# Optimization experiments

Measured on AMD Instinct MI355X. Metric: run time of the kernel, lower is better.

The kernel has to match this reference:

```python
import jax, jax.numpy as jnp
import numpy as np

EPS = 1e-12


def agnn_layer(x, row, col, num_nodes):
    """AGNN propagation with beta frozen at 1.0 (requires_grad=False in source).
    alpha_ij = softmax_{j in N(i)} ( beta * cos(x_i, x_j) ); out_i = sum_j alpha_ij * x_j.
    row = destination node of each edge (segment id), col = source node.
    """
    xn = x / (jnp.linalg.norm(x, axis=-1, keepdims=True) + EPS)  # unit-norm features
    score = jnp.sum(xn[row] * xn[col], axis=-1)                   # [E] beta=1 * cos sim
    smax = jax.ops.segment_max(score, row, num_segments=num_nodes)
    e = jnp.exp(score - smax[row])                                # stable softmax numerator
    denom = jax.ops.segment_sum(e, row, num_segments=num_nodes)
    alpha = e / jnp.maximum(denom[row], EPS)                      # [E]
    out = jax.ops.segment_sum(alpha[:, None] * x[col], row, num_segments=num_nodes)
    return out


def setup_inputs() -> dict:
    key = jax.random.key(0)
    ks = jax.random.split(key, 8)
    N, E = 100000, 1600000
    IN_DIM, HID, OUT_DIM = 128, 64, 64
    x = jax.random.normal(ks[0], (N, IN_DIM), dtype=jnp.float32)
    edge_row = jnp.sort(jax.random.randint(ks[1], (E,), 0, N))
    edge_col = jax.random.randint(ks[2], (E,), 0, N)
    # Linear params (PyTorch nn.Linear style: y = x @ W.T + b)
    s1 = 1.0 / np.sqrt(IN_DIM)
    W1 = jax.random.uniform(ks[3], (HID, IN_DIM), jnp.float32, -s1, s1)
    b1 = jax.random.uniform(ks[4], (HID,), jnp.float32, -s1, s1)
    s2 = 1.0 / np.sqrt(HID)
    W2 = jax.random.uniform(ks[5], (OUT_DIM, HID), jnp.float32, -s2, s2)
    b2 = jax.random.uniform(ks[6], (OUT_DIM,), jnp.float32, -s2, s2)
    return {"x": x, "edge_row": edge_row, "edge_col": edge_col,
            "W1": W1, "b1": b1, "W2": W2, "b2": b2}


def reference(x, edge_row, edge_col, W1, b1, W2, b2):
    N = x.shape[0]
    h = jax.nn.relu(x @ W1.T + b1)
    for _ in range(4):  # 4 frozen-beta AGNN layers
        h = jax.nn.relu(agnn_layer(h, edge_row, edge_col, N))
    return h @ W2.T + b2
```

## Files before the change

kernel.cpp:

```cpp
#include <hip/hip_runtime.h>


typedef float v2f __attribute__((ext_vector_type(2)));

#define DEV_INLINE __device__ __forceinline__

DEV_INLINE v2f bf2(unsigned u) {
    v2f r;
    r.x = __uint_as_float(u << 16);
    r.y = __uint_as_float(u & 0xffff0000u);
    return r;
}

DEV_INLINE unsigned pack_bf16_2(float a, float b) {
    unsigned ua = __float_as_uint(a); ua += 0x7fffu + ((ua >> 16) & 1u);
    unsigned ub = __float_as_uint(b); ub += 0x7fffu + ((ub >> 16) & 1u);
    return (ua >> 16) | (ub & 0xffff0000u);
}

__global__ __launch_bounds__(256) void build_rowptr(const int* __restrict__ row,
                                                    int* __restrict__ ptr,
                                                    int N, int E) {
    int i = blockIdx.x * blockDim.x + threadIdx.x;
    if (i > N) return;
    int lo = 0, hi = E;
    while (lo < hi) {
        int mid = (lo + hi) >> 1;
        if (row[mid] < i) lo = mid + 1; else hi = mid;
    }
    ptr[i] = lo;
}

__global__ __launch_bounds__(256) void gemm1_relu(const float* __restrict__ x,
                                                  const float* __restrict__ W1,
                                                  const float* __restrict__ b1,
                                                  unsigned short* __restrict__ xn,
                                                  float* __restrict__ nrm,
                                                  int N) {
    __shared__ __align__(16) float Wt[128 * 64];
    __shared__ __align__(16) float xT[128 * 64];
    const int tid  = threadIdx.x;
    const int tx   = tid & 15;
    const int ty   = tid >> 4;
    const int base = blockIdx.x * 64;

    {
        const float4* W4 = (const float4*)W1;
        for (int idx = tid; idx < 128 * 16; idx += 256) {
            int o = idx & 63, k4 = idx >> 6;
            float4 v = W4[o * 32 + k4];
            Wt[(4 * k4 + 0) * 64 + o] = v.x;
            Wt[(4 * k4 + 1) * 64 + o] = v.y;
            Wt[(4 * k4 + 2) * 64 + o] = v.z;
            Wt[(4 * k4 + 3) * 64 + o] = v.w;
        }
        const float4* x4p = (const float4*)x;
        for (int idx = tid; idx < 128 * 16; idx += 256) {
            int mm = idx & 63, k4 = idx >> 6;
            int node = base + mm;
            float4 v = make_float4(0.f, 0.f, 0.f, 0.f);
            if (node < N) v = x4p[(size_t)node * 32 + k4];
            xT[(4 * k4 + 0) * 64 + mm] = v.x;
            xT[(4 * k4 + 1) * 64 + mm] = v.y;
            xT[(4 * k4 + 2) * 64 + mm] = v.z;
            xT[(4 * k4 + 3) * 64 + mm] = v.w;
        }
    }
    __syncthreads();

    float4 b4 = ((const float4*)b1)[tx];
    float4 acc[4];
    acc[0] = b4; acc[1] = b4; acc[2] = b4; acc[3] = b4;

#pragma unroll 4
    for (int k = 0; k < 128; ++k) {
        const float4 w4 = *(const float4*)&Wt[k * 64 + 4 * tx];
        const float4 xv = *(const float4*)&xT[k * 64 + 4 * ty];
        acc[0].x = fmaf(xv.x, w4.x, acc[0].x);
        acc[0].y = fmaf(xv.x, w4.y, acc[0].y);
        acc[0].z = fmaf(xv.x, w4.z, acc[0].z);
        acc[0].w = fmaf(xv.x, w4.w, acc[0].w);
        acc[1].x = fmaf(xv.y, w4.x, acc[1].x);
        acc[1].y = fmaf(xv.y, w4.y, acc[1].y);
        acc[1].z = fmaf(xv.y, w4.z, acc[1].z);
        acc[1].w = fmaf(xv.y, w4.w, acc[1].w);
        acc[2].x = fmaf(xv.z, w4.x, acc[2].x);
        acc[2].y = fmaf(xv.z, w4.y, acc[2].y);
        acc[2].z = fmaf(xv.z, w4.z, acc[2].z);
        acc[2].w = fmaf(xv.z, w4.w, acc[2].w);
        acc[3].x = fmaf(xv.w, w4.x, acc[3].x);
        acc[3].y = fmaf(xv.w, w4.y, acc[3].y);
        acc[3].z = fmaf(xv.w, w4.z, acc[3].z);
        acc[3].w = fmaf(xv.w, w4.w, acc[3].w);
    }

#pragma unroll
    for (int mm = 0; mm < 4; ++mm) {
        float4 r = acc[mm];
        r.x = fmaxf(r.x, 0.f); r.y = fmaxf(r.y, 0.f);
        r.z = fmaxf(r.z, 0.f); r.w = fmaxf(r.w, 0.f);
        float s = fmaf(r.x, r.x, fmaf(r.y, r.y, fmaf(r.z, r.z, r.w * r.w)));
        s += __shfl_xor(s, 1, 64);
        s += __shfl_xor(s, 2, 64);
        s += __shfl_xor(s, 4, 64);
        s += __shfl_xor(s, 8, 64);
        const float nn  = sqrtf(s) + 1e-12f;
        const float inv = 1.f / nn;
        int node = base + 4 * ty + mm;
        if (node < N) {
            uint2 pk;
            pk.x = pack_bf16_2(r.x * inv, r.y * inv);
            pk.y = pack_bf16_2(r.z * inv, r.w * inv);
            *(uint2*)&xn[(size_t)node * 64 + 4 * tx] = pk;
            if (tx == mm) nrm[node] = nn;
        }
    }
}

__global__ __launch_bounds__(256) void agnn_layer(const uint4* __restrict__ xn4,
                                                  const float* __restrict__ nrm,
                                                  const int* __restrict__ ptr,
                                                  const int* __restrict__ col,
                                                  uint4* __restrict__ xo4,
                                                  float* __restrict__ nrmo,
                                                  int N) {
    const int tid  = threadIdx.x;
    const int lane = tid & 63;
    const int g    = (lane >> 3) & 3;
    const int sub  = lane & 7;
    const int i    = blockIdx.x * 8 + (tid >> 5);
    if (i >= N) return;

    const float L2E = 1.4426950408889634f;
    const uint4 hv = xn4[(size_t)i * 8 + sub];
    v2f hi0 = bf2(hv.x), hi1 = bf2(hv.y), hi2v = bf2(hv.z), hi3 = bf2(hv.w);
    hi0 *= L2E; hi1 *= L2E; hi2v *= L2E; hi3 *= L2E;

    const int p0 = ptr[i], p1 = ptr[i + 1];

    float den = 0.f;
    v2f a0 = {0.f, 0.f}, a1 = {0.f, 0.f}, a2 = {0.f, 0.f}, a3 = {0.f, 0.f};

    int e = p0 + g;
    for (; e + 4 < p1; e += 8) {
        const int ja = col[e];
        const int jb = col[e + 4];
        const uint4 va = xn4[(size_t)ja * 8 + sub];
        const uint4 vb = xn4[(size_t)jb * 8 + sub];
        const float na = nrm[ja];
        const float nb = nrm[jb];

        v2f x0 = bf2(va.x), x1 = bf2(va.y), x2 = bf2(va.z), x3 = bf2(va.w);
        v2f y0 = bf2(vb.x), y1 = bf2(vb.y), y2 = bf2(vb.z), y3 = bf2(vb.w);

        v2f sa2 = hi0 * x0; sa2 += hi1 * x1; sa2 += hi2v * x2; sa2 += hi3 * x3;
        v2f sb2 = hi0 * y0; sb2 += hi1 * y1; sb2 += hi2v * y2; sb2 += hi3 * y3;
        float sa = sa2.x + sa2.y;
        float sb = sb2.x + sb2.y;
        sa += __shfl_xor(sa, 1, 64);
        sb += __shfl_xor(sb, 1, 64);
        sa += __shfl_xor(sa, 2, 64);
        sb += __shfl_xor(sb, 2, 64);
        sa += __shfl_xor(sa, 4, 64);
        sb += __shfl_xor(sb, 4, 64);

        const float pa = exp2f(sa);
        const float pb = exp2f(sb);
        den += pa + pb;
        const float wa = pa * na;
        const float wb = pb * nb;
        v2f wa2 = {wa, wa}, wb2 = {wb, wb};
        a0 += wa2 * x0; a1 += wa2 * x1; a2 += wa2 * x2; a3 += wa2 * x3;
        a0 += wb2 * y0; a1 += wb2 * y1; a2 += wb2 * y2; a3 += wb2 * y3;
    }
    if (e < p1) {
        const int j = col[e];
        const uint4 v = xn4[(size_t)j * 8 + sub];
        const float nj = nrm[j];
        v2f x0 = bf2(v.x), x1 = bf2(v.y), x2 = bf2(v.z), x3 = bf2(v.w);
        v2f s2v = hi0 * x0; s2v += hi1 * x1; s2v += hi2v * x2; s2v += hi3 * x3;
        float s = s2v.x + s2v.y;
        s += __shfl_xor(s, 1, 64);
        s += __shfl_xor(s, 2, 64);
        s += __shfl_xor(s, 4, 64);
        const float p = exp2f(s);
        den += p;
        const float wp = p * nj;
        v2f w2 = {wp, wp};
        a0 += w2 * x0; a1 += w2 * x1; a2 += w2 * x2; a3 += w2 * x3;
    }

#pragma unroll
    for (int off = 8; off <= 16; off <<= 1) {
        den  += __shfl_xor(den, off, 64);
        a0.x += __shfl_xor(a0.x, off, 64);  a0.y += __shfl_xor(a0.y, off, 64);
        a1.x += __shfl_xor(a1.x, off, 64);  a1.y += __shfl_xor(a1.y, off, 64);
        a2.x += __shfl_xor(a2.x, off, 64);  a2.y += __shfl_xor(a2.y, off, 64);
        a3.x += __shfl_xor(a3.x, off, 64);  a3.y += __shfl_xor(a3.y, off, 64);
    }

    const float id = 1.f / fmaxf(den, 1e-12f);
    float o[8];
    o[0] = fmaxf(a0.x * id, 0.f); o[1] = fmaxf(a0.y * id, 0.f);
    o[2] = fmaxf(a1.x * id, 0.f); o[3] = fmaxf(a1.y * id, 0.f);
    o[4] = fmaxf(a2.x * id, 0.f); o[5] = fmaxf(a2.y * id, 0.f);
    o[6] = fmaxf(a3.x * id, 0.f); o[7] = fmaxf(a3.y * id, 0.f);

    float s2 = 0.f;
#pragma unroll
    for (int t = 0; t < 8; ++t) s2 = fmaf(o[t], o[t], s2);
    s2 += __shfl_xor(s2, 1, 64);
    s2 += __shfl_xor(s2, 2, 64);
    s2 += __shfl_xor(s2, 4, 64);
    const float nn  = sqrtf(s2) + 1e-12f;
    const float inv = 1.f / nn;

    if (g == 0) {
        uint4 ov;
        ov.x = pack_bf16_2(o[0] * inv, o[1] * inv);
        ov.y = pack_bf16_2(o[2] * inv, o[3] * inv);
        ov.z = pack_bf16_2(o[4] * inv, o[5] * inv);
        ov.w = pack_bf16_2(o[6] * inv, o[7] * inv);
        xo4[(size_t)i * 8 + sub] = ov;
        if (sub == 0) nrmo[i] = nn;
    }
}

__global__ __launch_bounds__(256) void gemm2(const unsigned short* __restrict__ xn,
                                             const float* __restrict__ nrm,
                                             const float* __restrict__ W2,
                                             const float* __restrict__ b2,
                                             float* __restrict__ out,
                                             int N) {
    __shared__ __align__(16) float Wt[64 * 64];
    __shared__ __align__(16) float xT[64 * 64];
    const int tid  = threadIdx.x;
    const int tx   = tid & 15;
    const int ty   = tid >> 4;
    const int base = blockIdx.x * 64;

    {
        const float4* W4 = (const float4*)W2;
        for (int idx = tid; idx < 64 * 16; idx += 256) {
            int o = idx & 63, k4 = idx >> 6;
            float4 v = W4[o * 16 + k4];
            Wt[(4 * k4 + 0) * 64 + o] = v.x;
            Wt[(4 * k4 + 1) * 64 + o] = v.y;
            Wt[(4 * k4 + 2) * 64 + o] = v.z;
            Wt[(4 * k4 + 3) * 64 + o] = v.w;
        }
        const uint2* x2 = (const uint2*)xn;
        for (int idx = tid; idx < 64 * 16; idx += 256) {
            int mm = idx & 63, k4 = idx >> 6;
            int node = base + mm;
            uint2 v = make_uint2(0u, 0u);
            float nn = 0.f;
            if (node < N) { v = x2[(size_t)node * 16 + k4]; nn = nrm[node]; }
            xT[(4 * k4 + 0) * 64 + mm] = __uint_as_float(v.x << 16) * nn;
            xT[(4 * k4 + 1) * 64 + mm] = __uint_as_float(v.x & 0xffff0000u) * nn;
            xT[(4 * k4 + 2) * 64 + mm] = __uint_as_float(v.y << 16) * nn;
            xT[(4 * k4 + 3) * 64 + mm] = __uint_as_float(v.y & 0xffff0000u) * nn;
        }
    }
    __syncthreads();

    float4 b4 = ((const float4*)b2)[tx];
    float4 acc[4];
    acc[0] = b4; acc[1] = b4; acc[2] = b4; acc[3] = b4;

#pragma unroll 4
    for (int k = 0; k < 64; ++k) {
        const float4 w4 = *(const float4*)&Wt[k * 64 + 4 * tx];
        const float4 xv = *(const float4*)&xT[k * 64 + 4 * ty];
        acc[0].x = fmaf(xv.x, w4.x, acc[0].x);
        acc[0].y = fmaf(xv.x, w4.y, acc[0].y);
        acc[0].z = fmaf(xv.x, w4.z, acc[0].z);
        acc[0].w = fmaf(xv.x, w4.w, acc[0].w);
        acc[1].x = fmaf(xv.y, w4.x, acc[1].x);
        acc[1].y = fmaf(xv.y, w4.y, acc[1].y);
        acc[1].z = fmaf(xv.y, w4.z, acc[1].z);
        acc[1].w = fmaf(xv.y, w4.w, acc[1].w);
        acc[2].x = fmaf(xv.z, w4.x, acc[2].x);
        acc[2].y = fmaf(xv.z, w4.y, acc[2].y);
        acc[2].z = fmaf(xv.z, w4.z, acc[2].z);
        acc[2].w = fmaf(xv.z, w4.w, acc[2].w);
        acc[3].x = fmaf(xv.w, w4.x, acc[3].x);
        acc[3].y = fmaf(xv.w, w4.y, acc[3].y);
        acc[3].z = fmaf(xv.w, w4.z, acc[3].z);
        acc[3].w = fmaf(xv.w, w4.w, acc[3].w);
    }

#pragma unroll
    for (int mm = 0; mm < 4; ++mm) {
        int node = base + 4 * ty + mm;
        if (node < N) *(float4*)&out[(size_t)node * 64 + 4 * tx] = acc[mm];
    }
}

extern "C" void kernel_launch(void* const* d_in, const int* in_sizes, int n_in,
                              void* d_out, int out_size, void* d_ws, size_t ws_size,
                              hipStream_t stream) {
    const float* x   = (const float*)d_in[0];
    const int*   row = (const int*)d_in[1];
    const int*   col = (const int*)d_in[2];
    const float* W1  = (const float*)d_in[3];
    const float* b1  = (const float*)d_in[4];
    const float* W2  = (const float*)d_in[5];
    const float* b2  = (const float*)d_in[6];
    float* out = (float*)d_out;

    const int N = in_sizes[0] / 128;
    const int E = in_sizes[1];

    char* ws = (char*)d_ws;
    size_t off = 0;
    unsigned short* ha = (unsigned short*)(ws + off); off += (size_t)N * 64 * 2;
    unsigned short* hb = (unsigned short*)(ws + off); off += (size_t)N * 64 * 2;
    float* na_ = (float*)(ws + off); off += (size_t)N * sizeof(float);
    float* nb_ = (float*)(ws + off); off += (size_t)N * sizeof(float);
    int*   ptr = (int*)  (ws + off); off += (size_t)(N + 1) * sizeof(int);
    (void)ws_size; (void)n_in; (void)out_size;

    build_rowptr<<<(N + 256) / 256, 256, 0, stream>>>(row, ptr, N, E);

    const int nbG = (N + 63) / 64;
    gemm1_relu<<<nbG, 256, 0, stream>>>(x, W1, b1, ha, na_, N);

    const int nb8 = (N + 7) / 8;
    unsigned short* hc = ha; unsigned short* hn = hb;
    float* nc = na_; float* nn = nb_;
    for (int l = 0; l < 4; ++l) {
        agnn_layer<<<nb8, 256, 0, stream>>>((const uint4*)hc, nc, ptr, col,
                                            (uint4*)hn, nn, N);
        unsigned short* t = hc; hc = hn; hn = t;
        float* tf = nc; nc = nn; nn = tf;
    }

    gemm2<<<nbG, 256, 0, stream>>>(hc, nc, W2, b2, out, N);
}
```

Measured before the change: 326.8 us.

## Use DPP group reductions, unroll edge loop by four, chunk GEMM LDS

The 8-lane dot-product reduction in the AGNN edge loop now uses DPP row-shift adds plus a ds_swizzle broadcast in place of three __shfl_xor calls, which shortens the per-edge reduction latency. The edge loop now issues four gathers per iteration instead of two, giving more memory-level parallelism, at the cost of more registers. The first GEMM splits K into two chunks of 64, halving its LDS footprint so more blocks can be resident, but it adds a barrier and reloads the tile. If the DPP and swizzle controls do not match the lane grouping, the scores would be wrong.

After: 336.6 us. 3.0% more time.

```diff
diff --git a/kernel.cpp b/kernel.cpp
--- a/kernel.cpp
+++ b/kernel.cpp
@@ -16,6 +16,18 @@
     unsigned ua = __float_as_uint(a); ua += 0x7fffu + ((ua >> 16) & 1u);
     unsigned ub = __float_as_uint(b); ub += 0x7fffu + ((ub >> 16) & 1u);
     return (ua >> 16) | (ub & 0xffff0000u);
+}
+
+template <int CTRL>
+DEV_INLINE float dpp_add(float v) {
+    int sh = __builtin_amdgcn_update_dpp(0, __float_as_int(v), CTRL, 0xF, 0xF, true);
+    return v + __int_as_float(sh);
+}
+DEV_INLINE float group8_sum_bcast(float v) {
+    float r = dpp_add<0x111>(v);
+    r = dpp_add<0x112>(r);
+    r = dpp_add<0x114>(r);
+    return __int_as_float(__builtin_amdgcn_ds_swizzle(__float_as_int(r), 0x00F8));
 }
 
 __global__ __launch_bounds__(256) void build_rowptr(const int* __restrict__ row,
@@ -37,61 +49,62 @@
                                                   unsigned short* __restrict__ xn,
                                                   float* __restrict__ nrm,
                                                   int N) {
-    __shared__ __align__(16) float Wt[128 * 64];
-    __shared__ __align__(16) float xT[128 * 64];
+    __shared__ __align__(16) float Wt[64 * 64];
+    __shared__ __align__(16) float xT[64 * 64];
     const int tid  = threadIdx.x;
     const int tx   = tid & 15;
     const int ty   = tid >> 4;
     const int base = blockIdx.x * 64;
 
-    {
+    float4 b4 = ((const float4*)b1)[tx];
+    float4 acc[4];
+    acc[0] = b4; acc[1] = b4; acc[2] = b4; acc[3] = b4;
+
+    for (int kc = 0; kc < 128; kc += 64) {
+        if (kc) __syncthreads();
         const float4* W4 = (const float4*)W1;
-        for (int idx = tid; idx < 128 * 16; idx += 256) {
+        for (int idx = tid; idx < 64 * 16; idx += 256) {
             int o = idx & 63, k4 = idx >> 6;
-            float4 v = W4[o * 32 + k4];
+            float4 v = W4[o * 32 + (kc >> 2) + k4];
             Wt[(4 * k4 + 0) * 64 + o] = v.x;
             Wt[(4 * k4 + 1) * 64 + o] = v.y;
             Wt[(4 * k4 + 2) * 64 + o] = v.z;
             Wt[(4 * k4 + 3) * 64 + o] = v.w;
         }
         const float4* x4p = (const float4*)x;
-        for (int idx = tid; idx < 128 * 16; idx += 256) {
+        for (int idx = tid; idx < 64 * 16; idx += 256) {
             int mm = idx & 63, k4 = idx >> 6;
             int node = base + mm;
             float4 v = make_float4(0.f, 0.f, 0.f, 0.f);
-            if (node < N) v = x4p[(size_t)node * 32 + k4];
+            if (node < N) v = x4p[(size_t)node * 32 + (kc >> 2) + k4];
             xT[(4 * k4 + 0) * 64 + mm] = v.x;
             xT[(4 * k4 + 1) * 64 + mm] = v.y;
             xT[(4 * k4 + 2) * 64 + mm] = v.z;
             xT[(4 * k4 + 3) * 64 + mm] = v.w;
         }
-    }
-    __syncthreads();
-
-    float4 b4 = ((const float4*)b1)[tx];
-    float4 acc[4];
-    acc[0] = b4; acc[1] = b4; acc[2] = b4; acc[3] = b4;
+        __syncthreads();
 
 #pragma unroll 4
-    for (int k = 0; k < 128; ++k) {
-        const float4 w4 = *(const float4*)&Wt[k * 64 + 4 * tx];
-        const float4 xv = *(const float4*)&xT[k * 64 + 4 * ty];
-        acc[0].x = fmaf(xv.x, w4.x, acc[0].x);
-        acc[0].y = fmaf(xv.x, w4.y, acc[0].y);
-        acc[0].z = fmaf(xv.x, w4.z, acc[0].z);
-        acc[0].w = fmaf(xv.x, w4.w, acc[0].w);
-        acc[1].x = fmaf(xv.y, w4.x, acc[1].x);
-        acc[1].y = fmaf(xv.y, w4.y, acc[1].y);
-        acc[1].z = fmaf(xv.y, w4.z, acc[1].z);
-        acc[1].w = fmaf(xv.y, w4.w, acc[1].w);
-        acc[2].x = fmaf(xv.z, w4.x, acc[2].x);
-        acc[2].y = fmaf(xv.z, w4.y, acc[2].y);
-        acc[2].z = fmaf(xv.z, w4.z, acc[2].z);
-        acc[2].w = fmaf(xv.z, w4.w, acc[2].w);
-        acc[3].x = fmaf(xv.w, w4.x, acc[3].x);
-        acc[3].y = fmaf(xv.w, w4.y, acc[3].y);
-        acc[3].z = fmaf(xv.w, w4.z, acc[3].z);
-        acc[3].w = fmaf(xv.w, w4.w, acc[3].w);
+        for (int k = 0; k < 64; ++k) {
+            const float4 w4 = *(const float4*)&Wt[k * 64 + 4 * tx];
+            const float4 xv = *(const float4*)&xT[k * 64 + 4 * ty];
+            acc[0].x = fmaf(xv.x, w4.x, acc[0].x);
+            acc[0].y = fmaf(xv.x, w4.y, acc[0].y);
+            acc[0].z = fmaf(xv.x, w4.z, acc[0].z);
+            acc[0].w = fmaf(xv.x, w4.w, acc[0].w);
+            acc[1].x = fmaf(xv.y, w4.x, acc[1].x);
+            acc[1].y = fmaf(xv.y, w4.y, acc[1].y);
+            acc[1].z = fmaf(xv.y, w4.z, acc[1].z);
+            acc[1].w = fmaf(xv.y, w4.w, acc[1].w);
+            acc[2].x = fmaf(xv.z, w4.x, acc[2].x);
+            acc[2].y = fmaf(xv.z, w4.y, acc[2].y);
+            acc[2].z = fmaf(xv.z, w4.z, acc[2].z);
+            acc[2].w = fmaf(xv.z, w4.w, acc[2].w);
+            acc[3].x = fmaf(xv.w, w4.x, acc[3].x);
+            acc[3].y = fmaf(xv.w, w4.y, acc[3].y);
+            acc[3].z = fmaf(xv.w, w4.z, acc[3].z);
+            acc[3].w = fmaf(xv.w, w4.w, acc[3].w);
+        }
     }
 
 #pragma unroll
@@ -141,54 +154,43 @@
     float den = 0.f;
     v2f a0 = {0.f, 0.f}, a1 = {0.f, 0.f}, a2 = {0.f, 0.f}, a3 = {0.f, 0.f};
 
+#define EDGE_BODY(V, NRMJ)                                                   \
+    {                                                                        \
+        v2f x0 = bf2((V).x), x1 = bf2((V).y), x2 = bf2((V).z), x3 = bf2((V).w); \
+        v2f s2v = hi0 * x0; s2v += hi1 * x1; s2v += hi2v * x2; s2v += hi3 * x3; \
+        const float p = exp2f(group8_sum_bcast(s2v.x + s2v.y));              \
+        den += p;                                                            \
+        const float wp = p * (NRMJ);                                         \
+        v2f w2 = {wp, wp};                                                   \
+        a0 += w2 * x0; a1 += w2 * x1; a2 += w2 * x2; a3 += w2 * x3;          \
+    }
+
     int e = p0 + g;
-    for (; e + 4 < p1; e += 8) {
-        const int ja = col[e];
-        const int jb = col[e + 4];
-        const uint4 va = xn4[(size_t)ja * 8 + sub];
-        const uint4 vb = xn4[(size_t)jb * 8 + sub];
-        const float na = nrm[ja];
-        const float nb = nrm[jb];
-
-        v2f x0 = bf2(va.x), x1 = bf2(va.y), x2 = bf2(va.z), x3 = bf2(va.w);
-        v2f y0 = bf2(vb.x), y1 = bf2(vb.y), y2 = bf2(vb.z), y3 = bf2(vb.w);
-
-        v2f sa2 = hi0 * x0; sa2 += hi1 * x1; sa2 += hi2v * x2; sa2 += hi3 * x3;
-        v2f sb2 = hi0 * y0; sb2 += hi1 * y1; sb2 += hi2v * y2; sb2 += hi3 * y3;
-        float sa = sa2.x + sa2.y;
-        float sb = sb2.x + sb2.y;
-        sa += __shfl_xor(sa, 1, 64);
-        sb += __shfl_xor(sb, 1, 64);
-        sa += __shfl_xor(sa, 2, 64);
-        sb += __shfl_xor(sb, 2, 64);
-        sa += __shfl_xor(sa, 4, 64);
-        sb += __shfl_xor(sb, 4, 64);
-
-        const float pa = exp2f(sa);
-        const float pb = exp2f(sb);
-        den += pa + pb;
-        const float wa = pa * na;
-        const float wb = pb * nb;
-        v2f wa2 = {wa, wa}, wb2 = {wb, wb};
-        a0 += wa2 * x0; a1 += wa2 * x1; a2 += wa2 * x2; a3 += wa2 * x3;
-        a0 += wb2 * y0; a1 += wb2 * y1; a2 += wb2 * y2; a3 += wb2 * y3;
-    }
-    if (e < p1) {
+    for (; e + 12 < p1; e += 16) {
+        const int j0 = col[e];
+        const int j1 = col[e + 4];
+        const int j2 = col[e + 8];
+        const int j3 = col[e + 12];
+        const uint4 v0 = xn4[(size_t)j0 * 8 + sub];
+        const uint4 v1 = xn4[(size_t)j1 * 8 + sub];
+        const uint4 v2 = xn4[(size_t)j2 * 8 + sub];
+        const uint4 v3 = xn4[(size_t)j3 * 8 + sub];
+        const float n0 = nrm[j0];
+        const float n1 = nrm[j1];
+        const float n2 = nrm[j2];
+        const float n3 = nrm[j3];
+        EDGE_BODY(v0, n0)
+        EDGE_BODY(v1, n1)
+        EDGE_BODY(v2, n2)
+        EDGE_BODY(v3, n3)
+    }
+    for (; e < p1; e += 4) {
         const int j = col[e];
         const uint4 v = xn4[(size_t)j * 8 + sub];
         const float nj = nrm[j];
-        v2f x0 = bf2(v.x), x1 = bf2(v.y), x2 = bf2(v.z), x3 = bf2(v.w);
-        v2f s2v = hi0 * x0; s2v += hi1 * x1; s2v += hi2v * x2; s2v += hi3 * x3;
-        float s = s2v.x + s2v.y;
-        s += __shfl_xor(s, 1, 64);
-        s += __shfl_xor(s, 2, 64);
-        s += __shfl_xor(s, 4, 64);
-        const float p = exp2f(s);
-        den += p;
-        const float wp = p * nj;
-        v2f w2 = {wp, wp};
-        a0 += w2 * x0; a1 += w2 * x1; a2 += w2 * x2; a3 += w2 * x3;
-    }
+        EDGE_BODY(v, nj)
+    }
+#undef EDGE_BODY
 
 #pragma unroll
     for (int off = 8; off <= 16; off <<= 1) {
```
